# Kernel optimization log

Hardware: AMD Instinct MI355X
Metric: run time of the kernel (lower is better)

Reference implementation:

```python
import jax, jax.numpy as jnp
import numpy as np

NEG = -9e15

def setup_inputs() -> dict:
    key = jax.random.key(0)
    k1, k2, k3, k4, k5 = jax.random.split(key, 5)
    N, Fin, Fout = 8192, 256, 128
    h = jax.random.normal(k1, (N, Fin), dtype=jnp.float32)
    adj = jax.random.randint(k2, (N, N), 0, 2, dtype=jnp.int32)
    # Parameters (xavier_uniform with gain=1.414 for a1/a2; kaiming-like for W is fine as random init)
    lim_w = float(np.sqrt(6.0 / (Fin + Fout)))
    W = jax.random.uniform(k3, (Fout, Fin), dtype=jnp.float32, minval=-lim_w, maxval=lim_w)
    lim_a = float(1.414 * np.sqrt(6.0 / (Fout + 1)))
    a1 = jax.random.uniform(k4, (Fout, 1), dtype=jnp.float32, minval=-lim_a, maxval=lim_a)
    a2 = jax.random.uniform(k5, (Fout, 1), dtype=jnp.float32, minval=-lim_a, maxval=lim_a)
    return {"h": h, "adj": adj, "W": W, "a1": a1, "a2": a2}

def reference(h, adj, W, a1, a2):
    Wh = h @ W.T                                   # [N, Fout]
    s1 = (Wh @ a1)                                 # [N, 1]
    s2 = (Wh @ a2)                                 # [N, 1]
    e = jax.nn.leaky_relu(s1 + s2.T, 0.2)          # [N, N]
    att = jnp.where(adj > 0, e, jnp.float32(NEG))
    att = jax.nn.softmax(att, axis=1)
    h_prime = att @ Wh                             # [N, Fout]
    return jax.nn.elu(h_prime)
```

## Files before the change

### kernel.cpp

```cpp
#include <hip/hip_runtime.h>
#include <cstdint>
#include <cstddef>

#define N_NODES 8192
#define FIN 256
#define FOUT 128
#define MT 32
#define KC 256
#define JS 4
#define JW (N_NODES / JS)
#define NCHS (JW / KC)
#define LOG2E 1.4426950408889634f

typedef __attribute__((ext_vector_type(8))) short bf16x8;
typedef __attribute__((ext_vector_type(4))) float f32x4;
typedef __attribute__((ext_vector_type(2))) unsigned int u32x2;

__device__ __forceinline__ float bf2f(unsigned short u) {
    union { unsigned int i; float f; } v; v.i = ((unsigned int)u) << 16; return v.f;
}
__device__ __forceinline__ unsigned short f2bf(float f) {
    union { float f; unsigned int i; } v; v.f = f;
    unsigned int r = (v.i + 0x7FFFu + ((v.i >> 16) & 1u)) >> 16;
    return (unsigned short)r;
}
__device__ __forceinline__ unsigned int pack_bf16(float a, float b) {
    return (unsigned)f2bf(a) | ((unsigned)f2bf(b) << 16);
}

__device__ __forceinline__ size_t whb_idx(int j, int f) {
    return ((size_t)((j >> 5) * 8 + (f >> 4)) << 9) + (((j >> 3) & 3) << 7)
         + ((f & 15) << 3) + (j & 7);
}

__global__ __launch_bounds__(256) void pack_kernel(const int* __restrict__ adj,
                                                   unsigned long long* __restrict__ bits) {
    const int t = threadIdx.x;
    const int lane = t & 63;
    const int wv = t >> 6;
    const int wid = blockIdx.x * 4 + wv;
#pragma unroll
    for (int pass = 0; pass < 2; ++pass) {
        const int row = wid + pass * 4096;
        const int* ar = adj + (size_t)row * N_NODES;
        unsigned long long k0 = 0, k1 = 0;
#pragma unroll
        for (int seg = 0; seg < 64; ++seg) {
            unsigned long long m = __ballot(ar[seg * 64 + lane] > 0);
            if (lane == seg) k0 = m;
        }
#pragma unroll
        for (int seg = 0; seg < 64; ++seg) {
            unsigned long long m = __ballot(ar[4096 + seg * 64 + lane] > 0);
            if (lane == seg) k1 = m;
        }
        unsigned long long* br = bits + (size_t)row * 128;
        br[lane] = k0;
        br[64 + lane] = k1;
    }
}

__global__ __launch_bounds__(256) void wh_kernel(const float* __restrict__ h,
                                                 const float* __restrict__ W,
                                                 unsigned short* __restrict__ whB) {
    __shared__ float hT[64][FIN + 5];
    const int t = threadIdx.x;
    const int i0 = blockIdx.x * 64;
    const int f0 = blockIdx.y * 32;
#pragma unroll
    for (int c = 0; c < 16; ++c) {
        int chunk = c * 256 + t;
        int row = chunk >> 6, col = (chunk & 63) * 4;
        f32x4 v = *(const f32x4*)&h[(size_t)(i0 + row) * FIN + col];
        hT[row][col] = v[0]; hT[row][col + 1] = v[1];
        hT[row][col + 2] = v[2]; hT[row][col + 3] = v[3];
    }
    __syncthreads();
    const int lane = t & 63;
    const int fb8 = __builtin_amdgcn_readfirstlane(f0 + (t >> 6) * 8);
    const float* w0 = W + (size_t)fb8 * FIN;
    float acc[8] = {0.f, 0.f, 0.f, 0.f, 0.f, 0.f, 0.f, 0.f};
    for (int k = 0; k < FIN; k += 4) {
        float h0 = hT[lane][k],     h1 = hT[lane][k + 1];
        float h2 = hT[lane][k + 2], h3 = hT[lane][k + 3];
#pragma unroll
        for (int c = 0; c < 8; ++c) {
            const float* wr = w0 + c * FIN;
            acc[c] += h0 * wr[k] + h1 * wr[k + 1] + h2 * wr[k + 2] + h3 * wr[k + 3];
        }
    }
    const int i = i0 + lane;
#pragma unroll
    for (int c = 0; c < 8; ++c)
        whB[whb_idx(i, fb8 + c)] = f2bf(acc[c]);
}

__global__ __launch_bounds__(256) void s_kernel(const unsigned short* __restrict__ whB,
                                                const float* __restrict__ a1,
                                                const float* __restrict__ a2,
                                                float* __restrict__ s1,
                                                float* __restrict__ s2) {
    __shared__ float p1[4][64], p2[4][64];
    const int t = threadIdx.x;
    const int l = t & 63;
    const int g = t >> 6;
    const int i = blockIdx.x * 64 + l;
    float acc1 = 0.f, acc2 = 0.f;
#pragma unroll
    for (int fb = g * 2; fb < g * 2 + 2; ++fb) {
#pragma unroll
        for (int sl = 0; sl < 16; ++sl) {
            int f = fb * 16 + sl;
            float v = bf2f(whB[whb_idx(i, f)]);
            acc1 += v * a1[f];
            acc2 += v * a2[f];
        }
    }
    p1[g][l] = acc1; p2[g][l] = acc2;
    __syncthreads();
    if (g == 0) {
        s1[i] = (p1[0][l] + p1[1][l] + p1[2][l] + p1[3][l]) * LOG2E;
        s2[i] = (p2[0][l] + p2[1][l] + p2[2][l] + p2[3][l]) * LOG2E;
    }
}

__global__ __launch_bounds__(256) void gat_kernel(const unsigned long long* __restrict__ bits,
                                                  const unsigned short* __restrict__ whB,
                                                  const float* __restrict__ s1,
                                                  const float* __restrict__ s2,
                                                  float* __restrict__ out,
                                                  float* __restrict__ nums,
                                                  float* __restrict__ dens) {
    __shared__ __align__(16) unsigned short sP[MT][KC + 8];
    __shared__ float sDen[MT];
    __shared__ float sS1[MT];
    const int t = threadIdx.x;
    const int slice = blockIdx.x & (JS - 1);
    const int i0 = (blockIdx.x >> 2) * MT;
    const int jb = slice * JW;
    const int kb0 = slice * (JW / 32);
    float* __restrict__ num = slice ? (nums + (size_t)(slice - 1) * N_NODES * FOUT) : out;
    float* __restrict__ den = dens + (size_t)slice * N_NODES;
    if (t < MT) { sDen[t] = 0.f; sS1[t] = s1[i0 + t]; }
    __syncthreads();

    const int r0 = t >> 4;
    const int s  = t & 15;
    const int lane = t & 63;
    const int quad = lane >> 4;
    const int sl = lane & 15;
    const int wv = t >> 6;
    const unsigned long long* bRow0 = bits + (size_t)(i0 + r0) * 128;
    const unsigned long long* bRow1 = bRow0 + (size_t)16 * 128;
    const int shft = (s & 3) * 16;
    const float s1a = sS1[r0];
    const float s1b = sS1[r0 + 16];

    f32x4 acc00 = {0.f,0.f,0.f,0.f}, acc01 = {0.f,0.f,0.f,0.f};
    f32x4 acc10 = {0.f,0.f,0.f,0.f}, acc11 = {0.f,0.f,0.f,0.f};

    int w0i = (jb >> 6) + (s >> 2);
    unsigned long long bw0 = bRow0[w0i];
    unsigned long long bw1 = bRow1[w0i];
    f32x4 sv[4];
#pragma unroll
    for (int q = 0; q < 4; ++q) sv[q] = *(const f32x4*)&s2[jb + s * 16 + q * 4];

    for (int ch = 0; ch < NCHS; ++ch) {
        unsigned int m0 = (unsigned int)(bw0 >> shft) & 0xFFFFu;
        unsigned int m1 = (unsigned int)(bw1 >> shft) & 0xFFFFu;
        float part0 = 0.f, part1 = 0.f;
#pragma unroll
        for (int q = 0; q < 4; ++q) {
            float p0[4], p1v[4];
#pragma unroll
            for (int r = 0; r < 4; ++r) {
                float y0 = s1a + sv[q][r];
                float y1 = s1b + sv[q][r];
                y0 = fmaxf(y0, 0.2f * y0);
                y1 = fmaxf(y1, 0.2f * y1);
                float e0 = __builtin_amdgcn_exp2f(y0);
                float e1 = __builtin_amdgcn_exp2f(y1);
                int b = q * 4 + r;
                p0[r]  = ((m0 >> b) & 1u) ? e0 : 0.f;
                p1v[r] = ((m1 >> b) & 1u) ? e1 : 0.f;
                part0 += p0[r];
                part1 += p1v[r];
            }
            u32x2 pk0, pk1;
            pk0.x = pack_bf16(p0[0], p0[1]);   pk0.y = pack_bf16(p0[2], p0[3]);
            pk1.x = pack_bf16(p1v[0], p1v[1]); pk1.y = pack_bf16(p1v[2], p1v[3]);
            *(u32x2*)&sP[r0][s * 16 + q * 4] = pk0;
            *(u32x2*)&sP[r0 + 16][s * 16 + q * 4] = pk1;
        }
        if (ch + 1 < NCHS) {
            int jn = jb + (ch + 1) * KC;
            int wni = (jn >> 6) + (s >> 2);
            bw0 = bRow0[wni];
            bw1 = bRow1[wni];
#pragma unroll
            for (int q = 0; q < 4; ++q) sv[q] = *(const f32x4*)&s2[jn + s * 16 + q * 4];
        }
        part0 += __shfl_xor(part0, 1); part1 += __shfl_xor(part1, 1);
        part0 += __shfl_xor(part0, 2); part1 += __shfl_xor(part1, 2);
        part0 += __shfl_xor(part0, 4); part1 += __shfl_xor(part1, 4);
        part0 += __shfl_xor(part0, 8); part1 += __shfl_xor(part1, 8);
        if (s == 0) { sDen[r0] += part0; sDen[r0 + 16] += part1; }
        __syncthreads();
#pragma unroll
        for (int kq = 0; kq < KC / 32; ++kq) {
            bf16x8 a0  = *(const bf16x8*)&sP[sl][kq * 32 + quad * 8];
            bf16x8 a1f = *(const bf16x8*)&sP[16 + sl][kq * 32 + quad * 8];
            int kb = kb0 + ch * (KC / 32) + kq;
            const unsigned short* t0 = whB + ((size_t)(kb * 8 + wv * 2) << 9) + lane * 8;
            bf16x8 b0 = *(const bf16x8*)t0;
            bf16x8 b1 = *(const bf16x8*)(t0 + 512);
            acc00 = __builtin_amdgcn_mfma_f32_16x16x32_bf16(a0,  b0, acc00, 0, 0, 0);
            acc01 = __builtin_amdgcn_mfma_f32_16x16x32_bf16(a0,  b1, acc01, 0, 0, 0);
            acc10 = __builtin_amdgcn_mfma_f32_16x16x32_bf16(a1f, b0, acc10, 0, 0, 0);
            acc11 = __builtin_amdgcn_mfma_f32_16x16x32_bf16(a1f, b1, acc11, 0, 0, 0);
        }
        __syncthreads();
    }
    if (t < MT) den[i0 + t] = sDen[t];
#pragma unroll
    for (int m = 0; m < 2; ++m) {
#pragma unroll
        for (int nn = 0; nn < 2; ++nn) {
            f32x4 a = (m == 0) ? (nn == 0 ? acc00 : acc01) : (nn == 0 ? acc10 : acc11);
#pragma unroll
            for (int r = 0; r < 4; ++r) {
                int row = m * 16 + quad * 4 + r;
                num[(size_t)(i0 + row) * FOUT + wv * 32 + nn * 16 + sl] = a[r];
            }
        }
    }
}

__global__ __launch_bounds__(256) void fin_kernel(float* __restrict__ out,
                                                  const float* __restrict__ nums,
                                                  const float* __restrict__ dens) {
    const int idx = blockIdx.x * 256 + threadIdx.x;
    const int i = idx >> 7;
    const size_t NF = (size_t)N_NODES * FOUT;
    float numv = out[idx] + nums[idx] + nums[NF + idx] + nums[2 * NF + idx];
    float denv = dens[i] + dens[N_NODES + i] + dens[2 * N_NODES + i] + dens[3 * N_NODES + i];
    float v = numv / fmaxf(denv, 1e-30f);
    out[idx] = (v > 0.f) ? v : expm1f(v);
}

extern "C" void kernel_launch(void* const* d_in, const int* in_sizes, int n_in,
                              void* d_out, int out_size, void* d_ws, size_t ws_size,
                              hipStream_t stream) {
    const float* h   = (const float*)d_in[0];
    const int*   adj = (const int*)d_in[1];
    const float* W   = (const float*)d_in[2];
    const float* a1  = (const float*)d_in[3];
    const float* a2  = (const float*)d_in[4];

    char* ws = (char*)d_ws;
    unsigned short*     whB  = (unsigned short*)ws;
    unsigned long long* bits = (unsigned long long*)(ws + (2u << 20));
    float* s1   = (float*)(ws + (10u << 20));
    float* s2   = s1 + N_NODES;
    float* dens = s2 + N_NODES;
    float* nums = dens + 4 * N_NODES;
    float* out  = (float*)d_out;

    pack_kernel<<<dim3(1024), 256, 0, stream>>>(adj, bits);
    wh_kernel<<<dim3(N_NODES / 64, FOUT / 32), 256, 0, stream>>>(h, W, whB);
    s_kernel<<<dim3(N_NODES / 64), 256, 0, stream>>>(whB, a1, a2, s1, s2);
    gat_kernel<<<dim3((N_NODES / MT) * JS), 256, 0, stream>>>(bits, whB, s1, s2,
                                                              out, nums, dens);
    fin_kernel<<<dim3(N_NODES * FOUT / 256), 256, 0, stream>>>(out, nums, dens);
}
```

Baseline: 433.2 us.

## Double row tile to 64 and split columns eight ways in GAT kernel

The attention kernel now handles 64 rows per block instead of 32, so each Wh B-fragment loaded from global memory feeds four MFMA row groups instead of two. The column dimension is split into 8 slices instead of 4 to keep enough blocks in flight, and the finalize kernel is generalized to reduce JS partial numerators and denominators. This trades more accumulator registers and a larger partial-sum workspace (7 extra N×F buffers read in the finalize pass) for less global traffic on Wh per unit of MFMA work. A launch bound hint of 4 blocks per CU is also added.

```diff
diff --git a/kernel.cpp b/kernel.cpp
--- a/kernel.cpp
+++ b/kernel.cpp
@@ -5,9 +5,9 @@
 #define N_NODES 8192
 #define FIN 256
 #define FOUT 128
-#define MT 32
+#define MT 64
 #define KC 256
-#define JS 4
+#define JS 8
 #define JW (N_NODES / JS)
 #define NCHS (JW / KC)
 #define LOG2E 1.4426950408889634f
@@ -124,19 +124,19 @@
     }
 }
 
-__global__ __launch_bounds__(256) void gat_kernel(const unsigned long long* __restrict__ bits,
-                                                  const unsigned short* __restrict__ whB,
-                                                  const float* __restrict__ s1,
-                                                  const float* __restrict__ s2,
-                                                  float* __restrict__ out,
-                                                  float* __restrict__ nums,
-                                                  float* __restrict__ dens) {
+__global__ __launch_bounds__(256, 4) void gat_kernel(const unsigned long long* __restrict__ bits,
+                                                     const unsigned short* __restrict__ whB,
+                                                     const float* __restrict__ s1,
+                                                     const float* __restrict__ s2,
+                                                     float* __restrict__ out,
+                                                     float* __restrict__ nums,
+                                                     float* __restrict__ dens) {
     __shared__ __align__(16) unsigned short sP[MT][KC + 8];
     __shared__ float sDen[MT];
     __shared__ float sS1[MT];
     const int t = threadIdx.x;
     const int slice = blockIdx.x & (JS - 1);
-    const int i0 = (blockIdx.x >> 2) * MT;
+    const int i0 = (blockIdx.x >> 3) * MT;
     const int jb = slice * JW;
     const int kb0 = slice * (JW / 32);
     float* __restrict__ num = slice ? (nums + (size_t)(slice - 1) * N_NODES * FOUT) : out;
@@ -150,88 +150,98 @@
     const int quad = lane >> 4;
     const int sl = lane & 15;
     const int wv = t >> 6;
-    const unsigned long long* bRow0 = bits + (size_t)(i0 + r0) * 128;
-    const unsigned long long* bRow1 = bRow0 + (size_t)16 * 128;
+    const unsigned long long* bR[4];
+    float s1r[4];
+#pragma unroll
+    for (int m = 0; m < 4; ++m) {
+        bR[m] = bits + (size_t)(i0 + r0 + 16 * m) * 128;
+        s1r[m] = sS1[r0 + 16 * m];
+    }
     const int shft = (s & 3) * 16;
-    const float s1a = sS1[r0];
-    const float s1b = sS1[r0 + 16];
-
-    f32x4 acc00 = {0.f,0.f,0.f,0.f}, acc01 = {0.f,0.f,0.f,0.f};
-    f32x4 acc10 = {0.f,0.f,0.f,0.f}, acc11 = {0.f,0.f,0.f,0.f};
-
-    int w0i = (jb >> 6) + (s >> 2);
-    unsigned long long bw0 = bRow0[w0i];
-    unsigned long long bw1 = bRow1[w0i];
+
+    f32x4 acc[4][2];
+#pragma unroll
+    for (int m = 0; m < 4; ++m) {
+        acc[m][0] = (f32x4){0.f, 0.f, 0.f, 0.f};
+        acc[m][1] = (f32x4){0.f, 0.f, 0.f, 0.f};
+    }
+
+    int wi = (jb >> 6) + (s >> 2);
+    unsigned long long bw[4];
+#pragma unroll
+    for (int m = 0; m < 4; ++m) bw[m] = bR[m][wi];
     f32x4 sv[4];
 #pragma unroll
     for (int q = 0; q < 4; ++q) sv[q] = *(const f32x4*)&s2[jb + s * 16 + q * 4];
 
     for (int ch = 0; ch < NCHS; ++ch) {
-        unsigned int m0 = (unsigned int)(bw0 >> shft) & 0xFFFFu;
-        unsigned int m1 = (unsigned int)(bw1 >> shft) & 0xFFFFu;
-        float part0 = 0.f, part1 = 0.f;
+        unsigned int mm[4];
+#pragma unroll
+        for (int m = 0; m < 4; ++m) mm[m] = (unsigned int)(bw[m] >> shft) & 0xFFFFu;
+        float part[4] = {0.f, 0.f, 0.f, 0.f};
 #pragma unroll
         for (int q = 0; q < 4; ++q) {
-            float p0[4], p1v[4];
-#pragma unroll
-            for (int r = 0; r < 4; ++r) {
-                float y0 = s1a + sv[q][r];
-                float y1 = s1b + sv[q][r];
-                y0 = fmaxf(y0, 0.2f * y0);
-                y1 = fmaxf(y1, 0.2f * y1);
-                float e0 = __builtin_amdgcn_exp2f(y0);
-                float e1 = __builtin_amdgcn_exp2f(y1);
-                int b = q * 4 + r;
-                p0[r]  = ((m0 >> b) & 1u) ? e0 : 0.f;
-                p1v[r] = ((m1 >> b) & 1u) ? e1 : 0.f;
-                part0 += p0[r];
-                part1 += p1v[r];
+#pragma unroll
+            for (int m = 0; m < 4; ++m) {
+                float p[4];
+#pragma unroll
+                for (int r = 0; r < 4; ++r) {
+                    float y = s1r[m] + sv[q][r];
+                    y = fmaxf(y, 0.2f * y);
+                    float e = __builtin_amdgcn_exp2f(y);
+                    p[r] = ((mm[m] >> (q * 4 + r)) & 1u) ? e : 0.f;
+                    part[m] += p[r];
+                }
+                u32x2 pk;
+                pk.x = pack_bf16(p[0], p[1]);
+                pk.y = pack_bf16(p[2], p[3]);
+                *(u32x2*)&sP[r0 + 16 * m][s * 16 + q * 4] = pk;
             }
-            u32x2 pk0, pk1;
-            pk0.x = pack_bf16(p0[0], p0[1]);   pk0.y = pack_bf16(p0[2], p0[3]);
-            pk1.x = pack_bf16(p1v[0], p1v[1]); pk1.y = pack_bf16(p1v[2], p1v[3]);
-            *(u32x2*)&sP[r0][s * 16 + q * 4] = pk0;
-            *(u32x2*)&sP[r0 + 16][s * 16 + q * 4] = pk1;
         }
         if (ch + 1 < NCHS) {
             int jn = jb + (ch + 1) * KC;
             int wni = (jn >> 6) + (s >> 2);
-            bw0 = bRow0[wni];
-            bw1 = bRow1[wni];
+#pragma unroll
+            for (int m = 0; m < 4; ++m) bw[m] = bR[m][wni];
 #pragma unroll
             for (int q = 0; q < 4; ++q) sv[q] = *(const f32x4*)&s2[jn + s * 16 + q * 4];
         }
-        part0 += __shfl_xor(part0, 1); part1 += __shfl_xor(part1, 1);
-        part0 += __shfl_xor(part0, 2); part1 += __shfl_xor(part1, 2);
-        part0 += __shfl_xor(part0, 4); part1 += __shfl_xor(part1, 4);
-        part0 += __shfl_xor(part0, 8); part1 += __shfl_xor(part1, 8);
-        if (s == 0) { sDen[r0] += part0; sDen[r0 + 16] += part1; }
+#pragma unroll
+        for (int m = 0; m < 4; ++m) {
+            part[m] += __shfl_xor(part[m], 1);
+            part[m] += __shfl_xor(part[m], 2);
+            part[m] += __shfl_xor(part[m], 4);
+            part[m] += __shfl_xor(part[m], 8);
+        }
+        if (s == 0) {
+#pragma unroll
+            for (int m = 0; m < 4; ++m) sDen[r0 + 16 * m] += part[m];
+        }
         __syncthreads();
 #pragma unroll
         for (int kq = 0; kq < KC / 32; ++kq) {
-            bf16x8 a0  = *(const bf16x8*)&sP[sl][kq * 32 + quad * 8];
-            bf16x8 a1f = *(const bf16x8*)&sP[16 + sl][kq * 32 + quad * 8];
             int kb = kb0 + ch * (KC / 32) + kq;
-            const unsigned short* t0 = whB + ((size_t)(kb * 8 + wv * 2) << 9) + lane * 8;
-            bf16x8 b0 = *(const bf16x8*)t0;
-            bf16x8 b1 = *(const bf16x8*)(t0 + 512);
-            acc00 = __builtin_amdgcn_mfma_f32_16x16x32_bf16(a0,  b0, acc00, 0, 0, 0);
-            acc01 = __builtin_amdgcn_mfma_f32_16x16x32_bf16(a0,  b1, acc01, 0, 0, 0);
-            acc10 = __builtin_amdgcn_mfma_f32_16x16x32_bf16(a1f, b0, acc10, 0, 0, 0);
-            acc11 = __builtin_amdgcn_mfma_f32_16x16x32_bf16(a1f, b1, acc11, 0, 0, 0);
+            const unsigned short* bp = whB + ((size_t)(kb * 8 + wv * 2) << 9) + lane * 8;
+            bf16x8 b0 = *(const bf16x8*)bp;
+            bf16x8 b1 = *(const bf16x8*)(bp + 512);
+#pragma unroll
+            for (int m = 0; m < 4; ++m) {
+                bf16x8 am = *(const bf16x8*)&sP[m * 16 + sl][kq * 32 + quad * 8];
+                acc[m][0] = __builtin_amdgcn_mfma_f32_16x16x32_bf16(am, b0, acc[m][0], 0, 0, 0);
+                acc[m][1] = __builtin_amdgcn_mfma_f32_16x16x32_bf16(am, b1, acc[m][1], 0, 0, 0);
+            }
         }
         __syncthreads();
     }
     if (t < MT) den[i0 + t] = sDen[t];
 #pragma unroll
-    for (int m = 0; m < 2; ++m) {
+    for (int m = 0; m < 4; ++m) {
 #pragma unroll
         for (int nn = 0; nn < 2; ++nn) {
-            f32x4 a = (m == 0) ? (nn == 0 ? acc00 : acc01) : (nn == 0 ? acc10 : acc11);
 #pragma unroll
             for (int r = 0; r < 4; ++r) {
                 int row = m * 16 + quad * 4 + r;
-                num[(size_t)(i0 + row) * FOUT + wv * 32 + nn * 16 + sl] = a[r];
+                num[(size_t)(i0 + row) * FOUT + wv * 32 + nn * 16 + sl] = acc[m][nn][r];
             }
         }
     }
@@ -243,8 +253,12 @@
     const int idx = blockIdx.x * 256 + threadIdx.x;
     const int i = idx >> 7;
     const size_t NF = (size_t)N_NODES * FOUT;
-    float numv = out[idx] + nums[idx] + nums[NF + idx] + nums[2 * NF + idx];
-    float denv = dens[i] + dens[N_NODES + i] + dens[2 * N_NODES + i] + dens[3 * N_NODES + i];
+    float numv = out[idx];
+#pragma unroll
+    for (int k = 0; k < JS - 1; ++k) numv += nums[k * NF + idx];
+    float denv = 0.f;
+#pragma unroll
+    for (int k = 0; k < JS; ++k) denv += dens[k * N_NODES + i];
     float v = numv / fmaxf(denv, 1e-30f);
     out[idx] = (v > 0.f) ? v : expm1f(v);
 }
@@ -264,7 +278,7 @@
     float* s1   = (float*)(ws + (10u << 20));
     float* s2   = s1 + N_NODES;
     float* dens = s2 + N_NODES;
-    float* nums = dens + 4 * N_NODES;
+    float* nums = dens + JS * N_NODES;
     float* out  = (float*)d_out;
 
     pack_kernel<<<dim3(1024), 256, 0, stream>>>(adj, bits);
```

New measurement: 458.1 us. 5.7% more time.

## Fuse adjacency read into GAT kernel and compute full-width tiles per wave in registers

Applied to the files above, without the earlier changes.

Drops the separate bit-packing kernel and has the attention kernel read the int32 adjacency directly, with prefetch one chunk ahead. Each wave now owns 32 rows and all 128 output features, so the probabilities feed the MFMA operands straight from registers with no shared-memory staging or block barriers. The column split goes from 4 to 8 slices to keep enough blocks. The cost is a wider per-wave accumulator (64 floats), more partial-sum traffic for the finalize kernel, and every block streaming the whole whB slice from global memory.

```diff
diff --git a/kernel.cpp b/kernel.cpp
--- a/kernel.cpp
+++ b/kernel.cpp
@@ -5,16 +5,14 @@
 #define N_NODES 8192
 #define FIN 256
 #define FOUT 128
-#define MT 32
-#define KC 256
-#define JS 4
+#define JS 8
 #define JW (N_NODES / JS)
-#define NCHS (JW / KC)
+#define KCH (JW / 32)
 #define LOG2E 1.4426950408889634f
 
 typedef __attribute__((ext_vector_type(8))) short bf16x8;
 typedef __attribute__((ext_vector_type(4))) float f32x4;
-typedef __attribute__((ext_vector_type(2))) unsigned int u32x2;
+typedef __attribute__((ext_vector_type(4))) int i32x4;
 
 __device__ __forceinline__ float bf2f(unsigned short u) {
     union { unsigned int i; float f; } v; v.i = ((unsigned int)u) << 16; return v.f;
@@ -31,33 +29,6 @@
 __device__ __forceinline__ size_t whb_idx(int j, int f) {
     return ((size_t)((j >> 5) * 8 + (f >> 4)) << 9) + (((j >> 3) & 3) << 7)
          + ((f & 15) << 3) + (j & 7);
-}
-
-__global__ __launch_bounds__(256) void pack_kernel(const int* __restrict__ adj,
-                                                   unsigned long long* __restrict__ bits) {
-    const int t = threadIdx.x;
-    const int lane = t & 63;
-    const int wv = t >> 6;
-    const int wid = blockIdx.x * 4 + wv;
-#pragma unroll
-    for (int pass = 0; pass < 2; ++pass) {
-        const int row = wid + pass * 4096;
-        const int* ar = adj + (size_t)row * N_NODES;
-        unsigned long long k0 = 0, k1 = 0;
-#pragma unroll
-        for (int seg = 0; seg < 64; ++seg) {
-            unsigned long long m = __ballot(ar[seg * 64 + lane] > 0);
-            if (lane == seg) k0 = m;
-        }
-#pragma unroll
-        for (int seg = 0; seg < 64; ++seg) {
-            unsigned long long m = __ballot(ar[4096 + seg * 64 + lane] > 0);
-            if (lane == seg) k1 = m;
-        }
-        unsigned long long* br = bits + (size_t)row * 128;
-        br[lane] = k0;
-        br[64 + lane] = k1;
-    }
 }
 
 __global__ __launch_bounds__(256) void wh_kernel(const float* __restrict__ h,
@@ -124,117 +95,108 @@
     }
 }
 
-__global__ __launch_bounds__(256) void gat_kernel(const unsigned long long* __restrict__ bits,
+__global__ __launch_bounds__(256) void gat_kernel(const int* __restrict__ adj,
                                                   const unsigned short* __restrict__ whB,
                                                   const float* __restrict__ s1,
                                                   const float* __restrict__ s2,
                                                   float* __restrict__ out,
                                                   float* __restrict__ nums,
                                                   float* __restrict__ dens) {
-    __shared__ __align__(16) unsigned short sP[MT][KC + 8];
-    __shared__ float sDen[MT];
-    __shared__ float sS1[MT];
     const int t = threadIdx.x;
+    const int w = t >> 6;
+    const int lane = t & 63;
+    const int sl = lane & 15;
+    const int quad = lane >> 4;
     const int slice = blockIdx.x & (JS - 1);
-    const int i0 = (blockIdx.x >> 2) * MT;
+    const int rg = (blockIdx.x >> 3) * 4 + w;
+    const int row0 = rg * 32;
     const int jb = slice * JW;
-    const int kb0 = slice * (JW / 32);
     float* __restrict__ num = slice ? (nums + (size_t)(slice - 1) * N_NODES * FOUT) : out;
     float* __restrict__ den = dens + (size_t)slice * N_NODES;
-    if (t < MT) { sDen[t] = 0.f; sS1[t] = s1[i0 + t]; }
-    __syncthreads();
-
-    const int r0 = t >> 4;
-    const int s  = t & 15;
-    const int lane = t & 63;
-    const int quad = lane >> 4;
-    const int sl = lane & 15;
-    const int wv = t >> 6;
-    const unsigned long long* bRow0 = bits + (size_t)(i0 + r0) * 128;
-    const unsigned long long* bRow1 = bRow0 + (size_t)16 * 128;
-    const int shft = (s & 3) * 16;
-    const float s1a = sS1[r0];
-    const float s1b = sS1[r0 + 16];
-
-    f32x4 acc00 = {0.f,0.f,0.f,0.f}, acc01 = {0.f,0.f,0.f,0.f};
-    f32x4 acc10 = {0.f,0.f,0.f,0.f}, acc11 = {0.f,0.f,0.f,0.f};
-
-    int w0i = (jb >> 6) + (s >> 2);
-    unsigned long long bw0 = bRow0[w0i];
-    unsigned long long bw1 = bRow1[w0i];
-    f32x4 sv[4];
-#pragma unroll
-    for (int q = 0; q < 4; ++q) sv[q] = *(const f32x4*)&s2[jb + s * 16 + q * 4];
-
-    for (int ch = 0; ch < NCHS; ++ch) {
-        unsigned int m0 = (unsigned int)(bw0 >> shft) & 0xFFFFu;
-        unsigned int m1 = (unsigned int)(bw1 >> shft) & 0xFFFFu;
-        float part0 = 0.f, part1 = 0.f;
+
+    const float s1a = s1[row0 + sl];
+    const float s1b = s1[row0 + 16 + sl];
+    const int* aR0 = adj + (size_t)(row0 + sl) * N_NODES + jb + quad * 8;
+    const int* aR1 = aR0 + (size_t)16 * N_NODES;
+    const float* s2p = s2 + jb + quad * 8;
+
+    f32x4 acc[2][8];
+#pragma unroll
+    for (int m = 0; m < 2; ++m)
+#pragma unroll
+        for (int fb = 0; fb < 8; ++fb) acc[m][fb] = (f32x4){0.f, 0.f, 0.f, 0.f};
+
+    float d0 = 0.f, d1 = 0.f;
+
+    i32x4 pa0 = *(const i32x4*)(aR0);
+    i32x4 pa1 = *(const i32x4*)(aR0 + 4);
+    i32x4 pb0 = *(const i32x4*)(aR1);
+    i32x4 pb1 = *(const i32x4*)(aR1 + 4);
+    f32x4 ps0 = *(const f32x4*)(s2p);
+    f32x4 ps1 = *(const f32x4*)(s2p + 4);
+
+#pragma unroll 1
+    for (int ch = 0; ch < KCH; ++ch) {
+        i32x4 ca0 = pa0, ca1 = pa1, cb0 = pb0, cb1 = pb1;
+        f32x4 cs0 = ps0, cs1 = ps1;
+        if (ch + 1 < KCH) {
+            int o = (ch + 1) * 32;
+            pa0 = *(const i32x4*)(aR0 + o);
+            pa1 = *(const i32x4*)(aR0 + o + 4);
+            pb0 = *(const i32x4*)(aR1 + o);
+            pb1 = *(const i32x4*)(aR1 + o + 4);
+            ps0 = *(const f32x4*)(s2p + o);
+            ps1 = *(const f32x4*)(s2p + o + 4);
+        }
+        const int kb = jb / 32 + ch;
+        const unsigned short* bp = whB + ((size_t)(kb * 8) << 9) + lane * 8;
+        bf16x8 B[8];
+#pragma unroll
+        for (int fb = 0; fb < 8; ++fb) B[fb] = *(const bf16x8*)(bp + ((size_t)fb << 9));
+        float p0[8], p1[8];
+#pragma unroll
+        for (int e = 0; e < 8; ++e) {
+            float sc = (e < 4) ? cs0[e] : cs1[e - 4];
+            int m0 = (e < 4) ? ca0[e] : ca1[e - 4];
+            int m1 = (e < 4) ? cb0[e] : cb1[e - 4];
+            float y0 = s1a + sc;
+            float y1 = s1b + sc;
+            y0 = fmaxf(y0, 0.2f * y0);
+            y1 = fmaxf(y1, 0.2f * y1);
+            float e0 = __builtin_amdgcn_exp2f(y0);
+            float e1 = __builtin_amdgcn_exp2f(y1);
+            p0[e] = (m0 > 0) ? e0 : 0.f;
+            p1[e] = (m1 > 0) ? e1 : 0.f;
+            d0 += p0[e];
+            d1 += p1[e];
+        }
+        union { bf16x8 v; unsigned int u[4]; } A0, A1;
 #pragma unroll
         for (int q = 0; q < 4; ++q) {
-            float p0[4], p1v[4];
+            A0.u[q] = pack_bf16(p0[2 * q], p0[2 * q + 1]);
+            A1.u[q] = pack_bf16(p1[2 * q], p1[2 * q + 1]);
+        }
+#pragma unroll
+        for (int fb = 0; fb < 8; ++fb) {
+            acc[0][fb] = __builtin_amdgcn_mfma_f32_16x16x32_bf16(A0.v, B[fb], acc[0][fb], 0, 0, 0);
+            acc[1][fb] = __builtin_amdgcn_mfma_f32_16x16x32_bf16(A1.v, B[fb], acc[1][fb], 0, 0, 0);
+        }
+    }
+    d0 += __shfl_xor(d0, 16); d0 += __shfl_xor(d0, 32);
+    d1 += __shfl_xor(d1, 16); d1 += __shfl_xor(d1, 32);
+    if (lane < 16) {
+        den[row0 + lane] = d0;
+        den[row0 + 16 + lane] = d1;
+    }
+#pragma unroll
+    for (int m = 0; m < 2; ++m)
+#pragma unroll
+        for (int fb = 0; fb < 8; ++fb)
 #pragma unroll
             for (int r = 0; r < 4; ++r) {
-                float y0 = s1a + sv[q][r];
-                float y1 = s1b + sv[q][r];
-                y0 = fmaxf(y0, 0.2f * y0);
-                y1 = fmaxf(y1, 0.2f * y1);
-                float e0 = __builtin_amdgcn_exp2f(y0);
-                float e1 = __builtin_amdgcn_exp2f(y1);
-                int b = q * 4 + r;
-                p0[r]  = ((m0 >> b) & 1u) ? e0 : 0.f;
-                p1v[r] = ((m1 >> b) & 1u) ? e1 : 0.f;
-                part0 += p0[r];
-                part1 += p1v[r];
+                int row = row0 + m * 16 + quad * 4 + r;
+                num[(size_t)row * FOUT + fb * 16 + sl] = acc[m][fb][r];
             }
-            u32x2 pk0, pk1;
-            pk0.x = pack_bf16(p0[0], p0[1]);   pk0.y = pack_bf16(p0[2], p0[3]);
-            pk1.x = pack_bf16(p1v[0], p1v[1]); pk1.y = pack_bf16(p1v[2], p1v[3]);
-            *(u32x2*)&sP[r0][s * 16 + q * 4] = pk0;
-            *(u32x2*)&sP[r0 + 16][s * 16 + q * 4] = pk1;
-        }
-        if (ch + 1 < NCHS) {
-            int jn = jb + (ch + 1) * KC;
-            int wni = (jn >> 6) + (s >> 2);
-            bw0 = bRow0[wni];
-            bw1 = bRow1[wni];
-#pragma unroll
-            for (int q = 0; q < 4; ++q) sv[q] = *(const f32x4*)&s2[jn + s * 16 + q * 4];
-        }
-        part0 += __shfl_xor(part0, 1); part1 += __shfl_xor(part1, 1);
-        part0 += __shfl_xor(part0, 2); part1 += __shfl_xor(part1, 2);
-        part0 += __shfl_xor(part0, 4); part1 += __shfl_xor(part1, 4);
-        part0 += __shfl_xor(part0, 8); part1 += __shfl_xor(part1, 8);
-        if (s == 0) { sDen[r0] += part0; sDen[r0 + 16] += part1; }
-        __syncthreads();
-#pragma unroll
-        for (int kq = 0; kq < KC / 32; ++kq) {
-            bf16x8 a0  = *(const bf16x8*)&sP[sl][kq * 32 + quad * 8];
-            bf16x8 a1f = *(const bf16x8*)&sP[16 + sl][kq * 32 + quad * 8];
-            int kb = kb0 + ch * (KC / 32) + kq;
-            const unsigned short* t0 = whB + ((size_t)(kb * 8 + wv * 2) << 9) + lane * 8;
-            bf16x8 b0 = *(const bf16x8*)t0;
-            bf16x8 b1 = *(const bf16x8*)(t0 + 512);
-            acc00 = __builtin_amdgcn_mfma_f32_16x16x32_bf16(a0,  b0, acc00, 0, 0, 0);
-            acc01 = __builtin_amdgcn_mfma_f32_16x16x32_bf16(a0,  b1, acc01, 0, 0, 0);
-            acc10 = __builtin_amdgcn_mfma_f32_16x16x32_bf16(a1f, b0, acc10, 0, 0, 0);
-            acc11 = __builtin_amdgcn_mfma_f32_16x16x32_bf16(a1f, b1, acc11, 0, 0, 0);
-        }
-        __syncthreads();
-    }
-    if (t < MT) den[i0 + t] = sDen[t];
-#pragma unroll
-    for (int m = 0; m < 2; ++m) {
-#pragma unroll
-        for (int nn = 0; nn < 2; ++nn) {
-            f32x4 a = (m == 0) ? (nn == 0 ? acc00 : acc01) : (nn == 0 ? acc10 : acc11);
-#pragma unroll
-            for (int r = 0; r < 4; ++r) {
-                int row = m * 16 + quad * 4 + r;
-                num[(size_t)(i0 + row) * FOUT + wv * 32 + nn * 16 + sl] = a[r];
-            }
-        }
-    }
 }
 
 __global__ __launch_bounds__(256) void fin_kernel(float* __restrict__ out,
@@ -243,8 +205,12 @@
     const int idx = blockIdx.x * 256 + threadIdx.x;
     const int i = idx >> 7;
     const size_t NF = (size_t)N_NODES * FOUT;
-    float numv = out[idx] + nums[idx] + nums[NF + idx] + nums[2 * NF + idx];
-    float denv = dens[i] + dens[N_NODES + i] + dens[2 * N_NODES + i] + dens[3 * N_NODES + i];
+    float numv = out[idx];
+#pragma unroll
+    for (int k = 0; k < JS - 1; ++k) numv += nums[k * NF + idx];
+    float denv = 0.f;
+#pragma unroll
+    for (int k = 0; k < JS; ++k) denv += dens[k * N_NODES + i];
     float v = numv / fmaxf(denv, 1e-30f);
     out[idx] = (v > 0.f) ? v : expm1f(v);
 }
@@ -259,18 +225,16 @@
     const float* a2  = (const float*)d_in[4];
 
     char* ws = (char*)d_ws;
-    unsigned short*     whB  = (unsigned short*)ws;
-    unsigned long long* bits = (unsigned long long*)(ws + (2u << 20));
-    float* s1   = (float*)(ws + (10u << 20));
+    unsigned short* whB = (unsigned short*)ws;
+    float* s1   = (float*)(ws + (2u << 20));
     float* s2   = s1 + N_NODES;
     float* dens = s2 + N_NODES;
-    float* nums = dens + 4 * N_NODES;
+    float* nums = dens + JS * N_NODES;
     float* out  = (float*)d_out;
 
-    pack_kernel<<<dim3(1024), 256, 0, stream>>>(adj, bits);
     wh_kernel<<<dim3(N_NODES / 64, FOUT / 32), 256, 0, stream>>>(h, W, whB);
     s_kernel<<<dim3(N_NODES / 64), 256, 0, stream>>>(whB, a1, a2, s1, s2);
-    gat_kernel<<<dim3((N_NODES / MT) * JS), 256, 0, stream>>>(bits, whB, s1, s2,
-                                                              out, nums, dens);
+    gat_kernel<<<dim3((N_NODES / 128) * JS), 256, 0, stream>>>(adj, whB, s1, s2,
+                                                               out, nums, dens);
     fin_kernel<<<dim3(N_NODES * FOUT / 256), 256, 0, stream>>>(out, nums, dens);
 }
```

New measurement: 446.1 us. 3.0% more time.
